# Optimization experiments

Hardware: AMD Instinct MI355X
Metric: run time of the kernel (lower is better)

Reference implementation:

```python
import jax, jax.numpy as jnp
import numpy as np

TOP_K = 8

def setup_inputs() -> dict:
    key = jax.random.key(0)
    k1, k2 = jax.random.split(key)
    N, D, E = 16384, 4096, 64
    x = jax.random.normal(k1, (N, D), dtype=jnp.float32)
    # xavier_uniform for Linear(D, E): weight shape (E, D), bound = sqrt(6/(D+E))
    bound = float(np.sqrt(6.0 / (D + E)))
    W = jax.random.uniform(k2, (E, D), dtype=jnp.float32, minval=-bound, maxval=bound)
    return {"x": x, "W": W}

def reference(x, W):
    # router logits: (N, E) = x @ W^T
    logits = jnp.einsum("nd,ed->ne", x, W)
    probs = jax.nn.softmax(logits, axis=-1)              # (N, E)
    top_k_probs, top_k_indices = jax.lax.top_k(probs, TOP_K)  # (N, K)
    gates = top_k_probs / (jnp.sum(top_k_probs, axis=-1, keepdims=True) + 1e-9)
    return gates, top_k_indices, probs
```

## Files before the change

kernel.cpp:

```cpp
#include <hip/hip_runtime.h>
#include <math.h>

#define NROWS 16384
#define DDIM  4096
#define NEXP  64
#define TOPK  8

#define BM   64
#define BK   16
#define NKT  (DDIM / BK)
#define LDP  68
#define LDPE 65


__global__ __launch_bounds__(256) void router_np(const float* __restrict__ x,
                                                 const float* __restrict__ W,
                                                 float* __restrict__ out) {
    __shared__ float As[2][BK][LDP];
    __shared__ float Bs[2][BK][LDP];
    __shared__ float lgs[BM][LDPE];

    const int t = threadIdx.x;
    const int block_row = blockIdx.x * BM;

    const int srow = t >> 2;
    const int sk   = (t & 3) * 4;

    const float* xa = x + (size_t)(block_row + srow) * DDIM + sk;
    const float* wb = W + (size_t)srow * DDIM + sk;

    const int tr = t >> 4;
    const int tc = t & 15;

    float acc[4][4][4];
    #pragma unroll
    for (int p = 0; p < 4; ++p)
        #pragma unroll
        for (int i = 0; i < 4; ++i)
            #pragma unroll
            for (int j = 0; j < 4; ++j) acc[p][i][j] = 0.f;

    {
        float4 a0 = *(const float4*)(xa);
        float4 b0 = *(const float4*)(wb);
        #pragma unroll
        for (int i = 0; i < 4; ++i) {
            As[0][sk + i][srow] = ((const float*)&a0)[i];
            Bs[0][sk + i][srow] = ((const float*)&b0)[i];
        }
    }

    auto compute_tile = [&](int bsel) {
        #pragma unroll
        for (int k = 0; k < BK; ++k) {
            float a[4], b[4];
            #pragma unroll
            for (int i = 0; i < 4; ++i) a[i] = As[bsel][k][tr * 4 + i];
            #pragma unroll
            for (int j = 0; j < 4; ++j) b[j] = Bs[bsel][k][tc * 4 + j];
            #pragma unroll
            for (int i = 0; i < 4; ++i)
                #pragma unroll
                for (int j = 0; j < 4; ++j)
                    acc[k & 3][i][j] =
                        __fadd_rn(acc[k & 3][i][j], __fmul_rn(a[i], b[j]));
        }
    };

    int buf = 0;
    for (int kt = 0; kt < NKT - 1; ++kt) {
        __syncthreads();
        const float* xn = xa + (size_t)(kt + 1) * BK;
        const float* wn = wb + (size_t)(kt + 1) * BK;
        float4 a0 = *(const float4*)(xn);
        float4 b0 = *(const float4*)(wn);

        compute_tile(buf);

        const int nb = buf ^ 1;
        #pragma unroll
        for (int i = 0; i < 4; ++i) {
            As[nb][sk + i][srow] = ((const float*)&a0)[i];
            Bs[nb][sk + i][srow] = ((const float*)&b0)[i];
        }
        buf = nb;
    }

    __syncthreads();
    compute_tile(buf);

    #pragma unroll
    for (int i = 0; i < 4; ++i)
        #pragma unroll
        for (int j = 0; j < 4; ++j)
            lgs[tr * 4 + i][tc * 4 + j] =
                __fadd_rn(__fadd_rn(acc[0][i][j], acc[1][i][j]),
                          __fadd_rn(acc[2][i][j], acc[3][i][j]));
    __syncthreads();

    float* out_gates = out;
    float* out_idx   = out + (size_t)NROWS * TOPK;
    float* out_probs = out + (size_t)NROWS * TOPK * 2;

    const int wave = t >> 6;
    const int lane = t & 63;

    for (int rr = 0; rr < BM / 4; ++rr) {
        const int row = wave * (BM / 4) + rr;
        const float l = lgs[row][lane];

        float m = l;
        #pragma unroll
        for (int off = 32; off > 0; off >>= 1)
            m = fmaxf(m, __shfl_xor(m, off));

        const float e = (float)exp((double)__fsub_rn(l, m));

        const int j8 = lane & 7;
        float r = __shfl(e, j8);
        #pragma unroll
        for (int s = 1; s < 8; ++s)
            r = __fadd_rn(r, __shfl(e, j8 + s * 8));
        const float r0 = __shfl(r, 0), r1 = __shfl(r, 1), r2 = __shfl(r, 2), r3 = __shfl(r, 3);
        const float r4 = __shfl(r, 4), r5 = __shfl(r, 5), r6 = __shfl(r, 6), r7 = __shfl(r, 7);
        const float S = __fadd_rn(__fadd_rn(__fadd_rn(r0, r1), __fadd_rn(r2, r3)),
                                  __fadd_rn(__fadd_rn(r4, r5), __fadd_rn(r6, r7)));

        const float prob = __fdiv_rn(e, S);

        const size_t grow = (size_t)(block_row + row);
        out_probs[grow * NEXP + lane] = prob;

        float work = prob;
        float myval = 0.f, topsum = 0.f;
        int   myidx = 0;
        for (int it = 0; it < TOPK; ++it) {
            float v = work;
            int   idx = lane;
            #pragma unroll
            for (int off = 32; off > 0; off >>= 1) {
                float ov = __shfl_xor(v, off);
                int   oi = __shfl_xor(idx, off);
                if (ov > v || (ov == v && oi < idx)) { v = ov; idx = oi; }
            }
            const float pw = __shfl(prob, idx);
            topsum = __fadd_rn(topsum, pw);
            if (lane == idx) work = -1.0f;
            if (lane == it)  { myval = pw; myidx = idx; }
        }
        if (lane < TOPK) {
            out_gates[grow * TOPK + lane] = __fdiv_rn(myval, __fadd_rn(topsum, 1e-9f));
            out_idx[grow * TOPK + lane]   = (float)myidx;
        }
    }
}

extern "C" void kernel_launch(void* const* d_in, const int* in_sizes, int n_in,
                              void* d_out, int out_size, void* d_ws, size_t ws_size,
                              hipStream_t stream) {
    const float* x = (const float*)d_in[0];
    const float* W = (const float*)d_in[1];
    float* out = (float*)d_out;

    dim3 grid(NROWS / BM);
    dim3 block(256);
    hipLaunchKernelGGL(router_np, grid, block, 0, stream, x, W, out);
}
```

Baseline: 242.1 us.

## Replace LDS-tiled router GEMM with register-only per-wave row dot products

Drops the shared-memory double-buffered 64x64 tile GEMM. Each wave now computes 4 rows, with each lane owning one expert and streaming its W row and the broadcast x rows through registers using two-stage software prefetching. This removes LDS traffic and block barriers. In exchange, every wave rereads the whole 1 MB W matrix, which raises cache traffic sharply, and the per-lane W loads are strided by a full row.

```diff
diff --git a/kernel.cpp b/kernel.cpp
--- a/kernel.cpp
+++ b/kernel.cpp
@@ -5,109 +5,73 @@
 #define DDIM  4096
 #define NEXP  64
 #define TOPK  8
-
-#define BM   64
-#define BK   16
-#define NKT  (DDIM / BK)
-#define LDP  68
-#define LDPE 65
+#define RPW   4
+#define CHUNK 8
 
 
-__global__ __launch_bounds__(256) void router_np(const float* __restrict__ x,
-                                                 const float* __restrict__ W,
-                                                 float* __restrict__ out) {
-    __shared__ float As[2][BK][LDP];
-    __shared__ float Bs[2][BK][LDP];
-    __shared__ float lgs[BM][LDPE];
+#define LOADC(kk, A0_, A1_, B0_, B1_) do {                                   \
+    _Pragma("unroll")                                                        \
+    for (int r_ = 0; r_ < RPW; ++r_) {                                       \
+        A0_[r_] = *(const float4*)(xr + (size_t)r_ * DDIM + (kk));           \
+        A1_[r_] = *(const float4*)(xr + (size_t)r_ * DDIM + (kk) + 4);       \
+    }                                                                        \
+    B0_ = *(const float4*)(wr + (kk));                                       \
+    B1_ = *(const float4*)(wr + (kk) + 4);                                   \
+} while (0)
 
-    const int t = threadIdx.x;
-    const int block_row = blockIdx.x * BM;
+#define COMPUTEC(A0_, A1_, B0_, B1_) do {                                    \
+    _Pragma("unroll")                                                        \
+    for (int r_ = 0; r_ < RPW; ++r_) {                                       \
+        s[r_][0] = __fadd_rn(s[r_][0], __fmul_rn(A0_[r_].x, B0_.x));         \
+        s[r_][1] = __fadd_rn(s[r_][1], __fmul_rn(A0_[r_].y, B0_.y));         \
+        s[r_][2] = __fadd_rn(s[r_][2], __fmul_rn(A0_[r_].z, B0_.z));         \
+        s[r_][3] = __fadd_rn(s[r_][3], __fmul_rn(A0_[r_].w, B0_.w));         \
+        s[r_][0] = __fadd_rn(s[r_][0], __fmul_rn(A1_[r_].x, B1_.x));         \
+        s[r_][1] = __fadd_rn(s[r_][1], __fmul_rn(A1_[r_].y, B1_.y));         \
+        s[r_][2] = __fadd_rn(s[r_][2], __fmul_rn(A1_[r_].z, B1_.z));         \
+        s[r_][3] = __fadd_rn(s[r_][3], __fmul_rn(A1_[r_].w, B1_.w));         \
+    }                                                                        \
+} while (0)
 
-    const int srow = t >> 2;
-    const int sk   = (t & 3) * 4;
+__global__ __launch_bounds__(256) void router_reg(const float* __restrict__ x,
+                                                  const float* __restrict__ W,
+                                                  float* __restrict__ out) {
+    const int lane = threadIdx.x & 63;
+    const int wv   = __builtin_amdgcn_readfirstlane((int)(threadIdx.x >> 6));
+    const int row0 = (blockIdx.x * 4 + wv) * RPW;
 
-    const float* xa = x + (size_t)(block_row + srow) * DDIM + sk;
-    const float* wb = W + (size_t)srow * DDIM + sk;
+    const float* xr = x + (size_t)row0 * DDIM;
+    const float* wr = W + (size_t)lane * DDIM;
 
-    const int tr = t >> 4;
-    const int tc = t & 15;
+    float s[RPW][4];
+    #pragma unroll
+    for (int r = 0; r < RPW; ++r)
+        #pragma unroll
+        for (int p = 0; p < 4; ++p) s[r][p] = 0.f;
 
-    float acc[4][4][4];
-    #pragma unroll
-    for (int p = 0; p < 4; ++p)
-        #pragma unroll
-        for (int i = 0; i < 4; ++i)
-            #pragma unroll
-            for (int j = 0; j < 4; ++j) acc[p][i][j] = 0.f;
+    float4 A0[RPW], A1[RPW], B0, B1;
+    float4 nA0[RPW], nA1[RPW], nB0, nB1;
 
-    {
-        float4 a0 = *(const float4*)(xa);
-        float4 b0 = *(const float4*)(wb);
-        #pragma unroll
-        for (int i = 0; i < 4; ++i) {
-            As[0][sk + i][srow] = ((const float*)&a0)[i];
-            Bs[0][sk + i][srow] = ((const float*)&b0)[i];
-        }
+    LOADC(0, A0, A1, B0, B1);
+    int k = 0;
+    for (; k + 2 * CHUNK < DDIM; k += 2 * CHUNK) {
+        LOADC(k + CHUNK, nA0, nA1, nB0, nB1);
+        COMPUTEC(A0, A1, B0, B1);
+        LOADC(k + 2 * CHUNK, A0, A1, B0, B1);
+        COMPUTEC(nA0, nA1, nB0, nB1);
     }
-
-    auto compute_tile = [&](int bsel) {
-        #pragma unroll
-        for (int k = 0; k < BK; ++k) {
-            float a[4], b[4];
-            #pragma unroll
-            for (int i = 0; i < 4; ++i) a[i] = As[bsel][k][tr * 4 + i];
-            #pragma unroll
-            for (int j = 0; j < 4; ++j) b[j] = Bs[bsel][k][tc * 4 + j];
-            #pragma unroll
-            for (int i = 0; i < 4; ++i)
-                #pragma unroll
-                for (int j = 0; j < 4; ++j)
-                    acc[k & 3][i][j] =
-                        __fadd_rn(acc[k & 3][i][j], __fmul_rn(a[i], b[j]));
-        }
-    };
-
-    int buf = 0;
-    for (int kt = 0; kt < NKT - 1; ++kt) {
-        __syncthreads();
-        const float* xn = xa + (size_t)(kt + 1) * BK;
-        const float* wn = wb + (size_t)(kt + 1) * BK;
-        float4 a0 = *(const float4*)(xn);
-        float4 b0 = *(const float4*)(wn);
-
-        compute_tile(buf);
-
-        const int nb = buf ^ 1;
-        #pragma unroll
-        for (int i = 0; i < 4; ++i) {
-            As[nb][sk + i][srow] = ((const float*)&a0)[i];
-            Bs[nb][sk + i][srow] = ((const float*)&b0)[i];
-        }
-        buf = nb;
-    }
-
-    __syncthreads();
-    compute_tile(buf);
-
-    #pragma unroll
-    for (int i = 0; i < 4; ++i)
-        #pragma unroll
-        for (int j = 0; j < 4; ++j)
-            lgs[tr * 4 + i][tc * 4 + j] =
-                __fadd_rn(__fadd_rn(acc[0][i][j], acc[1][i][j]),
-                          __fadd_rn(acc[2][i][j], acc[3][i][j]));
-    __syncthreads();
+    LOADC(k + CHUNK, nA0, nA1, nB0, nB1);
+    COMPUTEC(A0, A1, B0, B1);
+    COMPUTEC(nA0, nA1, nB0, nB1);
 
     float* out_gates = out;
     float* out_idx   = out + (size_t)NROWS * TOPK;
     float* out_probs = out + (size_t)NROWS * TOPK * 2;
 
-    const int wave = t >> 6;
-    const int lane = t & 63;
-
-    for (int rr = 0; rr < BM / 4; ++rr) {
-        const int row = wave * (BM / 4) + rr;
-        const float l = lgs[row][lane];
+    #pragma unroll
+    for (int r = 0; r < RPW; ++r) {
+        const float l = __fadd_rn(__fadd_rn(s[r][0], s[r][1]),
+                                  __fadd_rn(s[r][2], s[r][3]));
 
         float m = l;
         #pragma unroll
@@ -117,18 +81,20 @@
         const float e = (float)exp((double)__fsub_rn(l, m));
 
         const int j8 = lane & 7;
-        float r = __shfl(e, j8);
+        float rsum = __shfl(e, j8);
         #pragma unroll
-        for (int s = 1; s < 8; ++s)
-            r = __fadd_rn(r, __shfl(e, j8 + s * 8));
-        const float r0 = __shfl(r, 0), r1 = __shfl(r, 1), r2 = __shfl(r, 2), r3 = __shfl(r, 3);
-        const float r4 = __shfl(r, 4), r5 = __shfl(r, 5), r6 = __shfl(r, 6), r7 = __shfl(r, 7);
+        for (int t = 1; t < 8; ++t)
+            rsum = __fadd_rn(rsum, __shfl(e, j8 + t * 8));
+        const float r0 = __shfl(rsum, 0), r1 = __shfl(rsum, 1);
+        const float r2 = __shfl(rsum, 2), r3 = __shfl(rsum, 3);
+        const float r4 = __shfl(rsum, 4), r5 = __shfl(rsum, 5);
+        const float r6 = __shfl(rsum, 6), r7 = __shfl(rsum, 7);
         const float S = __fadd_rn(__fadd_rn(__fadd_rn(r0, r1), __fadd_rn(r2, r3)),
                                   __fadd_rn(__fadd_rn(r4, r5), __fadd_rn(r6, r7)));
 
         const float prob = __fdiv_rn(e, S);
 
-        const size_t grow = (size_t)(block_row + row);
+        const size_t grow = (size_t)(row0 + r);
         out_probs[grow * NEXP + lane] = prob;
 
         float work = prob;
@@ -162,7 +128,7 @@
     const float* W = (const float*)d_in[1];
     float* out = (float*)d_out;
 
-    dim3 grid(NROWS / BM);
+    dim3 grid(NROWS / (4 * RPW));
     dim3 block(256);
-    hipLaunchKernelGGL(router_np, grid, block, 0, stream, x, W, out);
+    hipLaunchKernelGGL(router_reg, grid, block, 0, stream, x, W, out);
 }
```

New measurement: 478.7 us. +97.8%, slower.
